# Kernel optimization log

Hardware: AMD Instinct MI355X
Metric: run time of the kernel (lower is better)

Reference implementation:

```python
import jax, jax.numpy as jnp
import numpy as np
import math

D_MODEL = 512
NUM_HEADS = 8
MAX_LEN = 10000.0


def positional_encoding_2d(seq_len, d_model, H, W, dtype=jnp.float32):
    # position along height repeated across width, and vice versa
    pos_h = jnp.repeat(jnp.arange(H, dtype=dtype), W)  # [H*W]
    pos_w = jnp.tile(jnp.arange(W, dtype=dtype), H)    # [H*W]
    div_term = jnp.exp(jnp.arange(0, d_model, 2, dtype=dtype) * (-(math.log(MAX_LEN) / d_model)))
    div = div_term[: d_model // 4]  # [d_model//4]
    pe = jnp.zeros((seq_len, d_model), dtype=dtype)
    pe = pe.at[:, 0::4].set(jnp.sin(pos_h[:, None] * div))
    pe = pe.at[:, 1::4].set(jnp.cos(pos_h[:, None] * div))
    pe = pe.at[:, 2::4].set(jnp.sin(pos_w[:, None] * div))
    pe = pe.at[:, 3::4].set(jnp.cos(pos_w[:, None] * div))
    return pe


def setup_inputs() -> dict:
    key = jax.random.key(0)
    ks = jax.random.split(key, 6)
    B, C, H, W = 8, D_MODEL, 32, 32
    d = D_MODEL
    s = 1.0 / math.sqrt(d)
    x = jax.random.normal(ks[0], (B, C, H, W), dtype=jnp.float32)
    Wq = jax.random.normal(ks[1], (d, d), dtype=jnp.float32) * s
    Wk = jax.random.normal(ks[2], (d, d), dtype=jnp.float32) * s
    Wv = jax.random.normal(ks[3], (d, d), dtype=jnp.float32) * s
    Wo = jax.random.normal(ks[4], (d, d), dtype=jnp.float32) * s
    bo = jnp.zeros((d,), dtype=jnp.float32)
    gamma = jnp.ones((d,), dtype=jnp.float32)
    beta = jnp.zeros((d,), dtype=jnp.float32)
    return {"x": x, "Wq": Wq, "Wk": Wk, "Wv": Wv, "Wo": Wo, "bo": bo, "gamma": gamma, "beta": beta}


def reference(x, Wq, Wk, Wv, Wo, bo, gamma, beta):
    B, C, H, W = x.shape
    d_model = C
    nh = NUM_HEADS
    dk = d_model // nh
    seq = H * W

    # [B, C, H, W] -> [B, seq, d_model]
    x_seq = x.reshape(B, C, seq).transpose(0, 2, 1)
    pe = positional_encoding_2d(seq, d_model, H, W, dtype=x.dtype)
    x_seq = x_seq + pe[None]
    residual = x_seq

    # QKV projections (torch Linear: y = x @ W.T)
    q = (x_seq @ Wq.T).reshape(B, seq, nh, dk).transpose(0, 2, 1, 3)  # [B, nh, S, dk]
    k = (x_seq @ Wk.T).reshape(B, seq, nh, dk).transpose(0, 2, 1, 3)
    v = (x_seq @ Wv.T).reshape(B, seq, nh, dk).transpose(0, 2, 1, 3)

    scores = jnp.einsum("bhsd,bhtd->bhst", q, k) / math.sqrt(dk)  # [B, nh, S, S]
    weights = jax.nn.softmax(scores, axis=-1)
    # dropout is identity at inference
    attn = jnp.einsum("bhst,bhtd->bhsd", weights, v)  # [B, nh, S, dk]
    attn = attn.transpose(0, 2, 1, 3).reshape(B, seq, d_model)

    out = attn @ Wo.T + bo
    y = out + residual
    mean = jnp.mean(y, axis=-1, keepdims=True)
    var = jnp.var(y, axis=-1, keepdims=True)
    y = (y - mean) / jnp.sqrt(var + 1e-5) * gamma + beta

    return y.transpose(0, 2, 1).reshape(B, C, H, W)
```

## Files before the change

### kernel.cpp

```cpp
#include <hip/hip_runtime.h>
#include <hip/hip_bf16.h>
#include <math.h>

#define DEV static __device__ __forceinline__

typedef unsigned short u16;
typedef unsigned int u32;
typedef __attribute__((ext_vector_type(4))) float f32x4;
typedef __attribute__((ext_vector_type(16))) float f32x16;
typedef __attribute__((ext_vector_type(8))) __bf16 bf16x8;
typedef __attribute__((ext_vector_type(4))) u16 u16x4;
typedef __attribute__((ext_vector_type(4))) u32 u32x4;

DEV u16 f2bf(float f) {
  unsigned u = __float_as_uint(f);
  u += 0x7fffu + ((u >> 16) & 1u);
  return (u16)(u >> 16);
}
DEV float bf2f(u16 x) { return __uint_as_float((u32)x << 16); }

DEV float fexp2(float x) { return __builtin_amdgcn_exp2f(x); }

DEV u32 cvt_pk_bf16(float lo, float hi) {
  u32 r;
  asm("v_cvt_pk_bf16_f32 %0, %1, %2" : "=v"(r) : "v"(lo), "v"(hi));
  return r;
}

DEV void perm32swap(u32& a, u32& b) {
  asm("v_permlane32_swap_b32 %0, %1" : "+v"(a), "+v"(b));
}

DEV void gl2lds16(const void* g, void* l) {
  __builtin_amdgcn_global_load_lds(
      (const __attribute__((address_space(1))) void*)g,
      (__attribute__((address_space(3))) void*)l, 16, 0, 0);
}

template<int RPW>
DEV void stage_rows(const u16* __restrict__ g, int gstride, u16* lds, int wave, int lane) {
  const int r_in = lane >> 3, slot = lane & 7;
  const int base_row = wave * RPW;
#pragma unroll
  for (int i = 0; i < RPW / 8; ++i) {
    const int row = base_row + i * 8 + r_in;
    const int sslot = slot ^ (row & 7);
    gl2lds16(g + (size_t)row * gstride + sslot * 8,
             lds + (size_t)(base_row + i * 8) * 64);
  }
}

DEV bf16x8 frag_read(const u16* lds, int row, int kslot) {
  const int slot = kslot ^ (row & 7);
  return *(const bf16x8*)(lds + row * 64 + slot * 8);
}

DEV f32x4 mfma16(bf16x8 a, bf16x8 b, f32x4 c) {
  return __builtin_amdgcn_mfma_f32_16x16x32_bf16(a, b, c, 0, 0, 0);
}
DEV f32x16 mfma32(bf16x8 a, bf16x8 b, f32x16 c) {
  return __builtin_amdgcn_mfma_f32_32x32x16_bf16(a, b, c, 0, 0, 0);
}

__global__ __launch_bounds__(256) void convert_w(
    const float* __restrict__ w0, const float* __restrict__ w1,
    const float* __restrict__ w2, const float* __restrict__ w3,
    u16* __restrict__ dst) {
  const float* src = (blockIdx.y == 0) ? w0 : (blockIdx.y == 1) ? w1
                   : (blockIdx.y == 2) ? w2 : w3;
  const size_t base = (size_t)blockIdx.y * 262144;
  const int i = (blockIdx.x * 256 + threadIdx.x) * 4;
  f32x4 v = *(const f32x4*)(src + i);
  u16x4 o;
  o.x = f2bf(v.x); o.y = f2bf(v.y); o.z = f2bf(v.z); o.w = f2bf(v.w);
  *(u16x4*)(dst + base + i) = o;
}

__global__ __launch_bounds__(256) void prep_x(
    const float* __restrict__ x, u16* __restrict__ Xp) {
  __shared__ float tile[32][33];
  const int b = blockIdx.z, c0 = blockIdx.y * 32, s0 = blockIdx.x * 32;
  const int t = threadIdx.x;
  const int cf = t >> 5, sf = t & 31;
#pragma unroll
  for (int i = 0; i < 4; ++i) {
    const int c = c0 + cf + i * 8;
    tile[cf + i * 8][sf] = x[((size_t)b * 512 + c) * 1024 + s0 + sf];
  }
  __syncthreads();
  const int cl = t & 31, sl = t >> 5;
  const int cg = c0 + cl;
  const int j = cg >> 2;
  const float dv = expf((float)j * (-9.210340371976184f / 256.0f));
#pragma unroll
  for (int i = 0; i < 4; ++i) {
    const int s = s0 + sl + i * 8;
    const float pos = (cg & 2) ? (float)(s & 31) : (float)(s >> 5);
    const float arg = pos * dv;
    const float pe = (cg & 1) ? cosf(arg) : sinf(arg);
    const float v = tile[cl][sl + i * 8] + pe;
    Xp[((size_t)b * 1024 + s) * 512 + cg] = f2bf(v);
  }
}

__global__ __launch_bounds__(256) void gemm_qkv(
    const u16* __restrict__ Xp, const u16* __restrict__ Wb,
    u16* __restrict__ Qb, u16* __restrict__ Kb, u16* __restrict__ Vtb,
    float qscale) {
  __shared__ __align__(16) u16 smem[128 * 132];
  u16* As = smem;
  u16* Bs = smem + 128 * 64;
  const int t = threadIdx.x, lane = t & 63, wave = t >> 6;
  const int bn0 = blockIdx.x * 128, bm0 = blockIdx.y * 128;
  const int wr = wave >> 1, wc = wave & 1;
  const u16* Ag = Xp + (size_t)bm0 * 512;
  const u16* Bg = Wb + (size_t)bn0 * 512;
  f32x4 acc[4][4] = {};
  for (int kt = 0; kt < 512; kt += 64) {
    __syncthreads();
    stage_rows<32>(Ag + kt, 512, As, wave, lane);
    stage_rows<32>(Bg + kt, 512, Bs, wave, lane);
    __syncthreads();
#pragma unroll
    for (int ks = 0; ks < 2; ++ks) {
      bf16x8 af[4], bfr[4];
#pragma unroll
      for (int m = 0; m < 4; ++m)
        af[m] = frag_read(As, wr * 64 + m * 16 + (lane & 15), ks * 4 + (lane >> 4));
#pragma unroll
      for (int n = 0; n < 4; ++n)
        bfr[n] = frag_read(Bs, wc * 64 + n * 16 + (lane & 15), ks * 4 + (lane >> 4));
#pragma unroll
      for (int m = 0; m < 4; ++m)
#pragma unroll
        for (int n = 0; n < 4; ++n)
          acc[m][n] = mfma16(af[m], bfr[n], acc[m][n]);
    }
  }
  const int cl = lane & 15, rg = (lane >> 4) * 4;
  if (bn0 >= 1024) {
    __syncthreads();
#pragma unroll
    for (int m = 0; m < 4; ++m)
#pragma unroll
      for (int n = 0; n < 4; ++n) {
        const int dvL = wc * 64 + n * 16 + cl;
        const int rowL0 = wr * 64 + m * 16 + rg;
        u16x4 pk;
#pragma unroll
        for (int r = 0; r < 4; ++r) pk[r] = f2bf(acc[m][n][r]);
        *(u16x4*)(smem + dvL * 132 + rowL0) = pk;
      }
    __syncthreads();
    const int dvg0 = bn0 - 1024;
#pragma unroll
    for (int i = 0; i < 16; ++i) {
      const int idx = i * 256 + t;
      const int dv = idx >> 5, ch = (idx & 31) * 4;
      const u16x4 v = *(const u16x4*)(smem + dv * 132 + ch);
      *(u16x4*)(Vtb + (size_t)(dvg0 + dv) * 8192 + bm0 + ch) = v;
    }
  } else {
    u16* dst = (bn0 >= 512) ? Kb : Qb;
    const float al = (bn0 >= 512) ? 1.0f : qscale;
    const int cb = (bn0 & 511) + wc * 64;
#pragma unroll
    for (int m = 0; m < 4; ++m)
#pragma unroll
      for (int n = 0; n < 4; ++n) {
        const int col = cb + n * 16 + cl;
#pragma unroll
        for (int r = 0; r < 4; ++r) {
          const int row = bm0 + wr * 64 + m * 16 + rg + r;
          dst[(size_t)row * 512 + col] = f2bf(acc[m][n][r] * al);
        }
      }
  }
}

__global__ __launch_bounds__(256) void gemm_ln(
    const u16* __restrict__ A, const u16* __restrict__ Bt,
    const u16* __restrict__ residb, const float* __restrict__ bias,
    const float* __restrict__ gamma, const float* __restrict__ beta,
    float* __restrict__ out) {
  __shared__ __align__(16) u16 smem[34816];
  __shared__ float redsum[4][32], redsq[4][32], srow[32][2];
  const int t = threadIdx.x, lane = t & 63, wave = t >> 6;
  const int m0 = blockIdx.x * 32;
  const int b = m0 >> 10, s0 = m0 & 1023;
  u16* As = smem;
  u16* Bs = smem + 2048;
  const u16* Ag = A + (size_t)m0 * 512;
  f32x4 acc[2][8] = {};
  for (int kt = 0; kt < 512; kt += 64) {
    __syncthreads();
    stage_rows<8>(Ag + kt, 512, As, wave, lane);
    stage_rows<128>(Bt + kt, 512, Bs, wave, lane);
    __syncthreads();
#pragma unroll
    for (int ks = 0; ks < 2; ++ks) {
      bf16x8 af[2], bfr[8];
#pragma unroll
      for (int m = 0; m < 2; ++m)
        af[m] = frag_read(As, m * 16 + (lane & 15), ks * 4 + (lane >> 4));
#pragma unroll
      for (int n = 0; n < 8; ++n)
        bfr[n] = frag_read(Bs, wave * 128 + n * 16 + (lane & 15), ks * 4 + (lane >> 4));
#pragma unroll
      for (int m = 0; m < 2; ++m)
#pragma unroll
        for (int n = 0; n < 8; ++n)
          acc[m][n] = mfma16(af[m], bfr[n], acc[m][n]);
    }
  }
  __syncthreads();
  float* fsm = (float*)smem;
  float* fw = fsm + wave * (128 * 33);
  const int cl = lane & 15, rg = (lane >> 4) * 4;
  float psum[8], psq[8];
#pragma unroll
  for (int i = 0; i < 8; ++i) { psum[i] = 0.f; psq[i] = 0.f; }
#pragma unroll
  for (int m = 0; m < 2; ++m)
#pragma unroll
    for (int n = 0; n < 8; ++n) {
      const int col_l = n * 16 + cl;
      const int col = wave * 128 + col_l;
      const float bi = bias[col];
#pragma unroll
      for (int r = 0; r < 4; ++r) {
        const int row_l = m * 16 + rg + r;
        const float v = acc[m][n][r] + bi
                      + bf2f(residb[(size_t)(m0 + row_l) * 512 + col]);
        fw[col_l * 33 + row_l] = v;
        psum[m * 4 + r] += v;
        psq[m * 4 + r] += v * v;
      }
    }
#pragma unroll
  for (int i = 0; i < 8; ++i) {
#pragma unroll
    for (int off = 8; off >= 1; off >>= 1) {
      psum[i] += __shfl_xor(psum[i], off);
      psq[i]  += __shfl_xor(psq[i], off);
    }
  }
  if (cl == 0) {
#pragma unroll
    for (int m = 0; m < 2; ++m)
#pragma unroll
      for (int r = 0; r < 4; ++r) {
        const int row_l = m * 16 + rg + r;
        redsum[wave][row_l] = psum[m * 4 + r];
        redsq[wave][row_l]  = psq[m * 4 + r];
      }
  }
  __syncthreads();
  if (t < 32) {
    float s = redsum[0][t] + redsum[1][t] + redsum[2][t] + redsum[3][t];
    float q = redsq[0][t] + redsq[1][t] + redsq[2][t] + redsq[3][t];
    const float mean = s * (1.f / 512.f);
    const float var = q * (1.f / 512.f) - mean * mean;
    srow[t][0] = mean;
    srow[t][1] = rsqrtf(var + 1e-5f);
  }
  __syncthreads();
  const int row = lane & 31, chalf = lane >> 5;
  const float mean = srow[row][0], rstd = srow[row][1];
  float* outb = out + (size_t)b * 512 * 1024 + s0 + row;
#pragma unroll 4
  for (int cc = 0; cc < 64; ++cc) {
    const int col_l = cc * 2 + chalf;
    const int col = wave * 128 + col_l;
    const float v = (fw[col_l * 33 + row] - mean) * rstd;
    outb[(size_t)col * 1024] = v * gamma[col] + beta[col];
  }
}

__global__ __launch_bounds__(256, 4) void attn(
    const u16* __restrict__ Qb, const u16* __restrict__ Kb,
    const u16* __restrict__ Vt, u16* __restrict__ Ob) {
  __shared__ __align__(16) u16 Ks[2][64 * 64];
  __shared__ __align__(16) u16 Vs[2][64 * 64];
  const int t = threadIdx.x, lane = t & 63, wave = t >> 6;
  const int wg = blockIdx.x;
  const int b = wg & 7, h = (wg >> 3) & 7, qt = wg >> 6;
  const int qsub = wave & 1, half = wave >> 1;
  const int ql = lane & 31, hl = lane >> 5;
  const int q0 = qt * 64 + qsub * 32;
  bf16x8 bq[4];
  {
    const u16* qrow = Qb + ((size_t)b * 1024 + q0 + ql) * 512 + h * 64 + hl * 8;
#pragma unroll
    for (int c = 0; c < 4; ++c) bq[c] = *(const bf16x8*)(qrow + c * 16);
  }
  f32x16 ot[2] = {};
  float m_run = -1e30f, l_run = 0.f;
  u16* stg_dst = qsub ? Vs[half] : Ks[half];
  for (int i = 0; i < 8; ++i) {
    const int kb = half * 512 + i * 64;
    {
      const int r_in = lane >> 3, slot = lane & 7;
      const u16* src; size_t gs;
      if (qsub) { src = Vt + (size_t)(h * 64) * 8192 + (size_t)b * 1024 + kb; gs = 8192; }
      else      { src = Kb + ((size_t)b * 1024 + kb) * 512 + h * 64;          gs = 512; }
#pragma unroll
      for (int j = 0; j < 8; ++j) {
        const int row = j * 8 + r_in;
        const int ss = slot ^ (row & 7);
        gl2lds16(src + (size_t)row * gs + ss * 8, stg_dst + j * 512);
      }
    }
    __syncthreads();
    f32x16 st[2] = {};
    __builtin_amdgcn_s_setprio(1);
#pragma unroll
    for (int c = 0; c < 4; ++c) {
      bf16x8 a0 = frag_read(Ks[half], ql, c * 2 + hl);
      bf16x8 a1 = frag_read(Ks[half], 32 + ql, c * 2 + hl);
      st[0] = mfma32(a0, bq[c], st[0]);
      st[1] = mfma32(a1, bq[c], st[1]);
    }
    __builtin_amdgcn_s_setprio(0);
    float m0[8];
#pragma unroll
    for (int i2 = 0; i2 < 8; ++i2)
      m0[i2] = fmaxf(fmaxf(st[0][i2], st[0][i2 + 8]), fmaxf(st[1][i2], st[1][i2 + 8]));
#pragma unroll
    for (int i2 = 0; i2 < 4; ++i2) m0[i2] = fmaxf(m0[i2], m0[i2 + 4]);
    float mx = fmaxf(fmaxf(m0[0], m0[1]), fmaxf(m0[2], m0[3]));
    mx = fmaxf(mx, __shfl_xor(mx, 32));
    if (!__all(mx <= m_run + 8.f)) {
      const float mn = fmaxf(m_run, mx);
      const float sc = fexp2(m_run - mn);
      m_run = mn;
      l_run *= sc;
      ot[0] *= sc;
      ot[1] *= sc;
    }
#pragma unroll
    for (int i2 = 0; i2 < 16; ++i2) {
      st[0][i2] = fexp2(st[0][i2] - m_run);
      st[1][i2] = fexp2(st[1][i2] - m_run);
    }
    float s0[8];
#pragma unroll
    for (int i2 = 0; i2 < 8; ++i2)
      s0[i2] = (st[0][i2] + st[0][i2 + 8]) + (st[1][i2] + st[1][i2 + 8]);
#pragma unroll
    for (int i2 = 0; i2 < 4; ++i2) s0[i2] = s0[i2] + s0[i2 + 4];
    float rs = (s0[0] + s0[1]) + (s0[2] + s0[3]);
    rs += __shfl_xor(rs, 32);
    l_run += rs;
    __builtin_amdgcn_s_setprio(1);
#pragma unroll
    for (int c = 0; c < 4; ++c) {
      const int kf = c >> 1, i0 = (c & 1) * 4;
      u32 w0 = cvt_pk_bf16(st[kf][2 * i0 + 0], st[kf][2 * i0 + 1]);
      u32 w1 = cvt_pk_bf16(st[kf][2 * i0 + 2], st[kf][2 * i0 + 3]);
      u32 w2 = cvt_pk_bf16(st[kf][2 * i0 + 4], st[kf][2 * i0 + 5]);
      u32 w3 = cvt_pk_bf16(st[kf][2 * i0 + 6], st[kf][2 * i0 + 7]);
      perm32swap(w0, w2);
      perm32swap(w1, w3);
      u32x4 wv; wv.x = w0; wv.y = w1; wv.z = w2; wv.w = w3;
      bf16x8 bp = *(bf16x8*)&wv;
      bf16x8 v0 = frag_read(Vs[half], ql, c * 2 + hl);
      bf16x8 v1 = frag_read(Vs[half], 32 + ql, c * 2 + hl);
      ot[0] = mfma32(v0, bp, ot[0]);
      ot[1] = mfma32(v1, bp, ot[1]);
    }
    __builtin_amdgcn_s_setprio(0);
    __syncthreads();
  }
  float* Om = (float*)&Ks[0][0] + qsub * 2048;
  float* Ml = (float*)&Vs[0][0];
  if (wave >= 2) {
#pragma unroll
    for (int df = 0; df < 2; ++df)
#pragma unroll
      for (int r = 0; r < 16; ++r) {
        const int dr = (r & 3) + 8 * (r >> 2) + 4 * hl;
        Om[(df * 32 + dr) * 32 + ql] = ot[df][r];
      }
    if (hl == 0) {
      Ml[qsub * 64 + ql] = m_run;
      Ml[qsub * 64 + 32 + ql] = l_run;
    }
    __syncthreads();
  } else {
    __syncthreads();
    const float m2 = Ml[qsub * 64 + ql];
    const float l2 = Ml[qsub * 64 + 32 + ql];
    const float m = fmaxf(m_run, m2);
    const float a = fexp2(m_run - m);
    const float bsc = fexp2(m2 - m);
    const float inv = 1.f / (l_run * a + l2 * bsc);
    u16* orow = Ob + ((size_t)b * 1024 + q0 + ql) * 512 + h * 64;
#pragma unroll
    for (int df = 0; df < 2; ++df)
#pragma unroll
      for (int r = 0; r < 16; ++r) {
        const int dr = (r & 3) + 8 * (r >> 2) + 4 * hl;
        const float v = ot[df][r] * a + Om[(df * 32 + dr) * 32 + ql] * bsc;
        orow[df * 32 + dr] = f2bf(v * inv);
      }
  }
}

extern "C" void kernel_launch(void* const* d_in, const int* in_sizes, int n_in,
                              void* d_out, int out_size, void* d_ws, size_t ws_size,
                              hipStream_t stream) {
  const float* x     = (const float*)d_in[0];
  const float* Wq    = (const float*)d_in[1];
  const float* Wk    = (const float*)d_in[2];
  const float* Wv    = (const float*)d_in[3];
  const float* Wo    = (const float*)d_in[4];
  const float* bo    = (const float*)d_in[5];
  const float* gamma = (const float*)d_in[6];
  const float* beta  = (const float*)d_in[7];
  char* ws = (char*)d_ws;
  const size_t MB = 1048576;
  u16*   Xp    = (u16*)(ws);
  u16*   Wb    = (u16*)(ws + 8 * MB);
  u16*   Qb    = (u16*)(ws + 10 * MB);
  u16*   Kb    = (u16*)(ws + 18 * MB);
  u16*   Vtb   = (u16*)(ws + 26 * MB);
  u16*   Ob    = (u16*)(ws + 34 * MB);

  convert_w<<<dim3(256, 4), 256, 0, stream>>>(Wq, Wk, Wv, Wo, Wb);
  prep_x<<<dim3(32, 16, 8), 256, 0, stream>>>(x, Xp);
  gemm_qkv<<<dim3(12, 64), 256, 0, stream>>>(Xp, Wb, Qb, Kb, Vtb,
                                             0.125f * 1.44269504088896f);
  attn<<<1024, 256, 0, stream>>>(Qb, Kb, Vtb, Ob);
  gemm_ln<<<256, 256, 0, stream>>>(Ob, Wb + 3 * 262144, Xp, bo, gamma, beta,
                                   (float*)d_out);
}
```

Baseline: 94.16 us.

## Pre-pack weights into MFMA fragment layout and read B operands from global

```diff
diff --git a/kernel.cpp b/kernel.cpp
--- a/kernel.cpp
+++ b/kernel.cpp
@@ -62,18 +62,26 @@
   return __builtin_amdgcn_mfma_f32_32x32x16_bf16(a, b, c, 0, 0, 0);
 }
 
-__global__ __launch_bounds__(256) void convert_w(
+__global__ __launch_bounds__(256) void pack_w(
     const float* __restrict__ w0, const float* __restrict__ w1,
     const float* __restrict__ w2, const float* __restrict__ w3,
     u16* __restrict__ dst) {
   const float* src = (blockIdx.y == 0) ? w0 : (blockIdx.y == 1) ? w1
                    : (blockIdx.y == 2) ? w2 : w3;
-  const size_t base = (size_t)blockIdx.y * 262144;
-  const int i = (blockIdx.x * 256 + threadIdx.x) * 4;
-  f32x4 v = *(const f32x4*)(src + i);
-  u16x4 o;
-  o.x = f2bf(v.x); o.y = f2bf(v.y); o.z = f2bf(v.z); o.w = f2bf(v.w);
-  *(u16x4*)(dst + base + i) = o;
+  const int lane = threadIdx.x & 63, wave = threadIdx.x >> 6;
+  const int c16 = blockIdx.x >> 2;
+  const int kchunk = (blockIdx.x & 3) * 4 + wave;
+  const int cl = lane & 15, ko = lane >> 4;
+  const float* s = src + (size_t)(c16 * 16 + cl) * 512 + kchunk * 32 + ko * 8;
+  const f32x4 a = *(const f32x4*)(s);
+  const f32x4 b = *(const f32x4*)(s + 4);
+  u16x4 lo, hi;
+#pragma unroll
+  for (int j = 0; j < 4; ++j) { lo[j] = f2bf(a[j]); hi[j] = f2bf(b[j]); }
+  u16* d = dst + (size_t)blockIdx.y * 262144
+               + (size_t)(c16 * 16 + kchunk) * 512 + lane * 8;
+  *(u16x4*)(d) = lo;
+  *(u16x4*)(d + 4) = hi;
 }
 
 __global__ __launch_bounds__(256) void prep_x(
@@ -104,32 +112,34 @@
 }
 
 __global__ __launch_bounds__(256) void gemm_qkv(
-    const u16* __restrict__ Xp, const u16* __restrict__ Wb,
+    const u16* __restrict__ Xp, const u16* __restrict__ Wpk,
     u16* __restrict__ Qb, u16* __restrict__ Kb, u16* __restrict__ Vtb,
     float qscale) {
   __shared__ __align__(16) u16 smem[128 * 132];
   u16* As = smem;
-  u16* Bs = smem + 128 * 64;
   const int t = threadIdx.x, lane = t & 63, wave = t >> 6;
   const int bn0 = blockIdx.x * 128, bm0 = blockIdx.y * 128;
   const int wr = wave >> 1, wc = wave & 1;
+  const int colbase = bn0 + wc * 64;
+  const int w = colbase >> 9;
+  const int cb16 = (colbase & 511) >> 4;
+  const u16* Bf = Wpk + (size_t)w * 262144;
   const u16* Ag = Xp + (size_t)bm0 * 512;
-  const u16* Bg = Wb + (size_t)bn0 * 512;
   f32x4 acc[4][4] = {};
   for (int kt = 0; kt < 512; kt += 64) {
     __syncthreads();
     stage_rows<32>(Ag + kt, 512, As, wave, lane);
-    stage_rows<32>(Bg + kt, 512, Bs, wave, lane);
     __syncthreads();
 #pragma unroll
     for (int ks = 0; ks < 2; ++ks) {
+      const int kc = (kt >> 5) + ks;
       bf16x8 af[4], bfr[4];
+#pragma unroll
+      for (int n = 0; n < 4; ++n)
+        bfr[n] = *(const bf16x8*)(Bf + (size_t)((cb16 + n) * 16 + kc) * 512 + lane * 8);
 #pragma unroll
       for (int m = 0; m < 4; ++m)
         af[m] = frag_read(As, wr * 64 + m * 16 + (lane & 15), ks * 4 + (lane >> 4));
-#pragma unroll
-      for (int n = 0; n < 4; ++n)
-        bfr[n] = frag_read(Bs, wc * 64 + n * 16 + (lane & 15), ks * 4 + (lane >> 4));
 #pragma unroll
       for (int m = 0; m < 4; ++m)
 #pragma unroll
@@ -179,7 +189,7 @@
 }
 
 __global__ __launch_bounds__(256) void gemm_ln(
-    const u16* __restrict__ A, const u16* __restrict__ Bt,
+    const u16* __restrict__ A, const u16* __restrict__ Wpk,
     const u16* __restrict__ residb, const float* __restrict__ bias,
     const float* __restrict__ gamma, const float* __restrict__ beta,
     float* __restrict__ out) {
@@ -189,23 +199,23 @@
   const int m0 = blockIdx.x * 32;
   const int b = m0 >> 10, s0 = m0 & 1023;
   u16* As = smem;
-  u16* Bs = smem + 2048;
+  const u16* Bf = Wpk + (size_t)3 * 262144;
   const u16* Ag = A + (size_t)m0 * 512;
   f32x4 acc[2][8] = {};
   for (int kt = 0; kt < 512; kt += 64) {
     __syncthreads();
     stage_rows<8>(Ag + kt, 512, As, wave, lane);
-    stage_rows<128>(Bt + kt, 512, Bs, wave, lane);
     __syncthreads();
 #pragma unroll
     for (int ks = 0; ks < 2; ++ks) {
+      const int kc = (kt >> 5) + ks;
       bf16x8 af[2], bfr[8];
+#pragma unroll
+      for (int n = 0; n < 8; ++n)
+        bfr[n] = *(const bf16x8*)(Bf + (size_t)((wave * 8 + n) * 16 + kc) * 512 + lane * 8);
 #pragma unroll
       for (int m = 0; m < 2; ++m)
         af[m] = frag_read(As, m * 16 + (lane & 15), ks * 4 + (lane >> 4));
-#pragma unroll
-      for (int n = 0; n < 8; ++n)
-        bfr[n] = frag_read(Bs, wave * 128 + n * 16 + (lane & 15), ks * 4 + (lane >> 4));
 #pragma unroll
       for (int m = 0; m < 2; ++m)
 #pragma unroll
@@ -421,17 +431,17 @@
   char* ws = (char*)d_ws;
   const size_t MB = 1048576;
   u16*   Xp    = (u16*)(ws);
-  u16*   Wb    = (u16*)(ws + 8 * MB);
+  u16*   Wpk   = (u16*)(ws + 8 * MB);
   u16*   Qb    = (u16*)(ws + 10 * MB);
   u16*   Kb    = (u16*)(ws + 18 * MB);
   u16*   Vtb   = (u16*)(ws + 26 * MB);
   u16*   Ob    = (u16*)(ws + 34 * MB);
 
-  convert_w<<<dim3(256, 4), 256, 0, stream>>>(Wq, Wk, Wv, Wo, Wb);
+  pack_w<<<dim3(128, 4), 256, 0, stream>>>(Wq, Wk, Wv, Wo, Wpk);
   prep_x<<<dim3(32, 16, 8), 256, 0, stream>>>(x, Xp);
-  gemm_qkv<<<dim3(12, 64), 256, 0, stream>>>(Xp, Wb, Qb, Kb, Vtb,
+  gemm_qkv<<<dim3(12, 64), 256, 0, stream>>>(Xp, Wpk, Qb, Kb, Vtb,
                                              0.125f * 1.44269504088896f);
   attn<<<1024, 256, 0, stream>>>(Qb, Kb, Vtb, Ob);
-  gemm_ln<<<256, 256, 0, stream>>>(Ob, Wb + 3 * 262144, Xp, bo, gamma, beta,
+  gemm_ln<<<256, 256, 0, stream>>>(Ob, Wpk, Xp, bo, gamma, beta,
                                    (float*)d_out);
 }
```

Result: no change. 94.09 us (-0.1%).
